# Kernel optimization log

Hardware: AMD Instinct MI355X
Metric: run time of the kernel (lower is better)

Reference implementation:

```python
import jax, jax.numpy as jnp
import numpy as np

N = 50000      # nodes
E = 800000     # edges
D_IN = 128
HID = 32
HEADS = 4
D_OUT = 64
NEG_SLOPE = 0.2  # DGL GATConv default


def gat_layer(feat, W, attn_l, attn_r, bias, src, dst, H, F):
    """One DGL-style GATConv layer. feat:[N,in], W:[in,H*F], attn:[H,F], bias:[H*F]."""
    n = feat.shape[0]
    hp = (feat @ W).reshape(n, H, F)                      # projected features [N,H,F]
    el = jnp.sum(hp * attn_l, axis=-1)                    # [N,H]
    er = jnp.sum(hp * attn_r, axis=-1)                    # [N,H]
    e = jax.nn.leaky_relu(el[src] + er[dst], NEG_SLOPE)   # per-edge score [E,H]
    # segment softmax over incoming edges of each dst node
    m = jax.ops.segment_max(e, dst, num_segments=n)       # [N,H]
    a = jnp.exp(e - m[dst])
    denom = jax.ops.segment_sum(a, dst, num_segments=n)   # [N,H]
    alpha = a / denom[dst]                                # [E,H]
    msg = alpha[:, :, None] * hp[src]                     # [E,H,F]
    out = jax.ops.segment_sum(msg, dst, num_segments=n)   # [N,H,F]
    return out + bias.reshape(1, H, F)


def setup_inputs() -> dict:
    key = jax.random.key(0)
    ks = jax.random.split(key, 12)
    s = 0.05
    x = jax.random.normal(ks[0], (N, D_IN), dtype=jnp.float32)
    src = jax.random.randint(ks[1], (E,), 0, N)
    dst = jax.random.randint(ks[2], (E,), 0, N)
    # layer 1: D_IN -> HID with HEADS heads
    W1 = jax.random.normal(ks[3], (D_IN, HEADS * HID), dtype=jnp.float32) * s
    al1 = jax.random.normal(ks[4], (HEADS, HID), dtype=jnp.float32) * s
    ar1 = jax.random.normal(ks[5], (HEADS, HID), dtype=jnp.float32) * s
    b1 = jnp.zeros((HEADS * HID,), dtype=jnp.float32)
    # layer 2: HID*HEADS -> D_OUT with 1 head
    W2 = jax.random.normal(ks[6], (HID * HEADS, D_OUT), dtype=jnp.float32) * s
    al2 = jax.random.normal(ks[7], (1, D_OUT), dtype=jnp.float32) * s
    ar2 = jax.random.normal(ks[8], (1, D_OUT), dtype=jnp.float32) * s
    b2 = jnp.zeros((D_OUT,), dtype=jnp.float32)
    return {"x": x, "W1": W1, "al1": al1, "ar1": ar1, "b1": b1,
            "W2": W2, "al2": al2, "ar2": ar2, "b2": b2,
            "src": src, "dst": dst}


def reference(x, W1, al1, ar1, b1, W2, al2, ar2, b2, src, dst):
    h1 = gat_layer(x, W1, al1, ar1, b1, src, dst, HEADS, HID)   # [N,HEADS,HID]
    h1 = h1.reshape(N, HEADS * HID)                              # concat heads
    h2 = gat_layer(h1, W2, al2, ar2, b2, src, dst, 1, D_OUT)     # [N,1,D_OUT]
    return h2.reshape(N, D_OUT)                                  # squeeze head dim
```

## Files before the change

kernel.cpp:

```cpp
#include <hip/hip_runtime.h>

#define NEG_SLOPE 0.2f

static __device__ __forceinline__ unsigned short f2bf(float f) {
  unsigned x = __float_as_uint(f);
  return (unsigned short)((x + 0x7FFFu + ((x >> 16) & 1u)) >> 16);
}
static __device__ __forceinline__ float bf2f(unsigned short u) {
  return __uint_as_float((unsigned)u << 16);
}

template<int NCOLS, int H>
__global__ __launch_bounds__(256) void gemm_eler_rank(const float* __restrict__ A,
    const float* __restrict__ B, const float* __restrict__ al, const float* __restrict__ ar,
    unsigned short* __restrict__ hb, float* __restrict__ el, float* __restrict__ er, int M,
    int gemmBlocks, const int* __restrict__ dst, int* deg, int* __restrict__ rank, int E) {
  constexpr int K = 128;
  constexpr int TM = 64;
  constexpr int F = NCOLS / H;
  __shared__ float As[TM][K];
  const int tid = threadIdx.x;

  if (blockIdx.x >= gemmBlocks) {
    const int e = (blockIdx.x - gemmBlocks) * 256 + tid;
    if (e < E) rank[e] = atomicAdd(&deg[dst[e]], 1);
    return;
  }

  const int m0 = blockIdx.x * TM;
  for (int i = tid; i < TM * K / 4; i += 256) {
    const int m = (i * 4) / K, k = (i * 4) % K;
    float4 v = make_float4(0.f, 0.f, 0.f, 0.f);
    if (m0 + m < M) v = *reinterpret_cast<const float4*>(&A[(size_t)(m0 + m) * K + k]);
    *reinterpret_cast<float4*>(&As[m][k]) = v;
  }
  __syncthreads();

  constexpr int CW = NCOLS / 32;
  const int c0 = (tid & 31) * CW;
  const int n0 = (tid >> 5) * 8;
  float acc[8][CW];
  #pragma unroll
  for (int i = 0; i < 8; ++i)
    #pragma unroll
    for (int j = 0; j < CW; ++j) acc[i][j] = 0.f;

  #pragma unroll 4
  for (int k = 0; k < K; ++k) {
    float wv[CW];
    if constexpr (CW == 4)
      *reinterpret_cast<float4*>(&wv[0]) = *reinterpret_cast<const float4*>(&B[(size_t)k * NCOLS + c0]);
    else
      *reinterpret_cast<float2*>(&wv[0]) = *reinterpret_cast<const float2*>(&B[(size_t)k * NCOLS + c0]);
    float xv[8];
    #pragma unroll
    for (int i = 0; i < 8; ++i) xv[i] = As[n0 + i][k];
    #pragma unroll
    for (int i = 0; i < 8; ++i)
      #pragma unroll
      for (int j = 0; j < CW; ++j)
        acc[i][j] = fmaf(xv[i], wv[j], acc[i][j]);
  }

  float alv[CW], arv[CW];
  if constexpr (CW == 4) {
    *reinterpret_cast<float4*>(&alv[0]) = *reinterpret_cast<const float4*>(&al[c0]);
    *reinterpret_cast<float4*>(&arv[0]) = *reinterpret_cast<const float4*>(&ar[c0]);
  } else {
    *reinterpret_cast<float2*>(&alv[0]) = *reinterpret_cast<const float2*>(&al[c0]);
    *reinterpret_cast<float2*>(&arv[0]) = *reinterpret_cast<const float2*>(&ar[c0]);
  }
  constexpr int GRP = F / CW;
  const int h = c0 / F;

  #pragma unroll
  for (int i = 0; i < 8; ++i) {
    const int m = m0 + n0 + i;
    if (m < M) {
      if constexpr (CW == 4) {
        ushort4 u;
        u.x = f2bf(acc[i][0]); u.y = f2bf(acc[i][1]);
        u.z = f2bf(acc[i][2]); u.w = f2bf(acc[i][3]);
        *reinterpret_cast<ushort4*>(&hb[(size_t)m * NCOLS + c0]) = u;
      } else {
        ushort2 u;
        u.x = f2bf(acc[i][0]); u.y = f2bf(acc[i][1]);
        *reinterpret_cast<ushort2*>(&hb[(size_t)m * NCOLS + c0]) = u;
      }
    }
    float pl = 0.f, pr = 0.f;
    #pragma unroll
    for (int j = 0; j < CW; ++j) {
      pl = fmaf(alv[j], acc[i][j], pl);
      pr = fmaf(arv[j], acc[i][j], pr);
    }
    #pragma unroll
    for (int off = 1; off < GRP; off <<= 1) {
      pl += __shfl_xor(pl, off);
      pr += __shfl_xor(pr, off);
    }
    if (((tid & 31) & (GRP - 1)) == 0 && m < M) {
      el[(size_t)m * H + h] = pl;
      er[(size_t)m * H + h] = pr;
    }
  }
}

__global__ __launch_bounds__(256) void block_sum_kernel(const int* __restrict__ deg,
    int* __restrict__ partials, int N) {
  __shared__ int wsum[4];
  const int tid = threadIdx.x;
  const int base = blockIdx.x * 1024 + tid * 4;
  int s = 0;
  #pragma unroll
  for (int j = 0; j < 4; ++j) if (base + j < N) s += deg[base + j];
  #pragma unroll
  for (int off = 32; off >= 1; off >>= 1) s += __shfl_down(s, off);
  if ((tid & 63) == 0) wsum[tid >> 6] = s;
  __syncthreads();
  if (tid == 0) partials[blockIdx.x] = wsum[0] + wsum[1] + wsum[2] + wsum[3];
}

__global__ __launch_bounds__(64) void scan_partials_kernel(int* partials, int nb) {
  const int tid = threadIdx.x;
  int v = (tid < nb) ? partials[tid] : 0;
  int incl = v;
  #pragma unroll
  for (int off = 1; off < 64; off <<= 1) {
    const int t = __shfl_up(incl, off);
    if (tid >= off) incl += t;
  }
  if (tid < nb) partials[tid] = incl - v;
}

__global__ __launch_bounds__(256) void block_scan_kernel(const int* __restrict__ deg,
    const int* __restrict__ partials, int* __restrict__ row_ptr, int N, int E) {
  __shared__ int wtot[4];
  const int tid = threadIdx.x;
  const int lane = tid & 63, wid = tid >> 6;
  const int idx = blockIdx.x * 1024 + tid * 4;
  int v[4];
  #pragma unroll
  for (int j = 0; j < 4; ++j) v[j] = (idx + j < N) ? deg[idx + j] : 0;
  const int tsum = v[0] + v[1] + v[2] + v[3];
  int incl = tsum;
  #pragma unroll
  for (int off = 1; off < 64; off <<= 1) {
    const int t = __shfl_up(incl, off);
    if (lane >= off) incl += t;
  }
  if (lane == 63) wtot[wid] = incl;
  __syncthreads();
  int excl = partials[blockIdx.x] + incl - tsum;
  for (int w = 0; w < wid; ++w) excl += wtot[w];
  #pragma unroll
  for (int j = 0; j < 4; ++j) {
    if (idx + j < N) { row_ptr[idx + j] = excl; excl += v[j]; }
  }
  if (blockIdx.x == 0 && tid == 0) row_ptr[N] = E;
}

__global__ __launch_bounds__(256) void place_kernel(const int* __restrict__ src,
    const int* __restrict__ dst, const int* __restrict__ row_ptr,
    const int* __restrict__ rank, unsigned short* __restrict__ csr_src, int E) {
  const int e = blockIdx.x * 256 + threadIdx.x;
  if (e < E) {
    csr_src[row_ptr[dst[e]] + rank[e]] = (unsigned short)src[e];
  }
}

template<int H, int F, int NPW>
__global__ __launch_bounds__(256) void gat_agg(const int* __restrict__ row_ptr,
    const unsigned short* __restrict__ csr_src, const float* __restrict__ el,
    const float* __restrict__ er, const unsigned short* __restrict__ hb,
    const float* __restrict__ bias, float* __restrict__ out, int N) {
  constexpr int HF = H * F;
  constexpr int LPN = 64 / NPW;
  constexpr int CPL = HF / LPN;
  static_assert(CPL == 4, "CPL must be 4");
  const int wid = threadIdx.x >> 6;
  const int lane = threadIdx.x & 63;
  const int g = lane / LPN;
  const int gl = lane % LPN;
  const int d = (blockIdx.x * 4 + wid) * NPW + g;
  if (d >= N) return;
  const int c0 = gl * CPL;
  const int h = c0 / F;
  const float erd = er[(size_t)d * H + h];
  const int beg = row_ptr[d], end = row_ptr[d + 1];
  float a0 = 0.f, a1 = 0.f, a2 = 0.f, a3 = 0.f, denom = 0.f;
  int i = beg;

  for (; i + 16 <= end; i += 16) {
    int s[16];
    #pragma unroll
    for (int j = 0; j < 16; ++j) s[j] = csr_src[i + j];
    float ee[16];
    #pragma unroll
    for (int j = 0; j < 16; ++j) ee[j] = el[(size_t)s[j] * H + h];
    ushort4 u[16];
    #pragma unroll
    for (int j = 0; j < 16; ++j)
      u[j] = *reinterpret_cast<const ushort4*>(&hb[(size_t)s[j] * HF + c0]);
    #pragma unroll
    for (int j = 0; j < 16; ++j) {
      float t = ee[j] + erd;
      t = fmaxf(t, NEG_SLOPE * t);
      const float x = __expf(t);
      denom += x;
      a0 = fmaf(x, bf2f(u[j].x), a0); a1 = fmaf(x, bf2f(u[j].y), a1);
      a2 = fmaf(x, bf2f(u[j].z), a2); a3 = fmaf(x, bf2f(u[j].w), a3);
    }
  }
  for (; i + 8 <= end; i += 8) {
    int s[8];
    #pragma unroll
    for (int j = 0; j < 8; ++j) s[j] = csr_src[i + j];
    float ee[8];
    #pragma unroll
    for (int j = 0; j < 8; ++j) ee[j] = el[(size_t)s[j] * H + h];
    ushort4 u[8];
    #pragma unroll
    for (int j = 0; j < 8; ++j)
      u[j] = *reinterpret_cast<const ushort4*>(&hb[(size_t)s[j] * HF + c0]);
    #pragma unroll
    for (int j = 0; j < 8; ++j) {
      float t = ee[j] + erd;
      t = fmaxf(t, NEG_SLOPE * t);
      const float x = __expf(t);
      denom += x;
      a0 = fmaf(x, bf2f(u[j].x), a0); a1 = fmaf(x, bf2f(u[j].y), a1);
      a2 = fmaf(x, bf2f(u[j].z), a2); a3 = fmaf(x, bf2f(u[j].w), a3);
    }
  }
  for (; i + 4 <= end; i += 4) {
    int s[4];
    #pragma unroll
    for (int j = 0; j < 4; ++j) s[j] = csr_src[i + j];
    float ee[4];
    #pragma unroll
    for (int j = 0; j < 4; ++j) ee[j] = el[(size_t)s[j] * H + h];
    ushort4 u[4];
    #pragma unroll
    for (int j = 0; j < 4; ++j)
      u[j] = *reinterpret_cast<const ushort4*>(&hb[(size_t)s[j] * HF + c0]);
    #pragma unroll
    for (int j = 0; j < 4; ++j) {
      float t = ee[j] + erd;
      t = fmaxf(t, NEG_SLOPE * t);
      const float x = __expf(t);
      denom += x;
      a0 = fmaf(x, bf2f(u[j].x), a0); a1 = fmaf(x, bf2f(u[j].y), a1);
      a2 = fmaf(x, bf2f(u[j].z), a2); a3 = fmaf(x, bf2f(u[j].w), a3);
    }
  }
  for (; i < end; ++i) {
    const int s = csr_src[i];
    float t = el[(size_t)s * H + h] + erd;
    t = fmaxf(t, NEG_SLOPE * t);
    const float x = __expf(t);
    denom += x;
    const ushort4 u = *reinterpret_cast<const ushort4*>(&hb[(size_t)s * HF + c0]);
    a0 = fmaf(x, bf2f(u.x), a0); a1 = fmaf(x, bf2f(u.y), a1);
    a2 = fmaf(x, bf2f(u.z), a2); a3 = fmaf(x, bf2f(u.w), a3);
  }

  const float inv = denom > 0.f ? 1.f / denom : 0.f;
  const float4 bv = *reinterpret_cast<const float4*>(&bias[c0]);
  float4 o;
  o.x = bv.x + a0 * inv; o.y = bv.y + a1 * inv;
  o.z = bv.z + a2 * inv; o.w = bv.w + a3 * inv;
  *reinterpret_cast<float4*>(&out[(size_t)d * HF + c0]) = o;
}

extern "C" void kernel_launch(void* const* d_in, const int* in_sizes, int n_in,
                              void* d_out, int out_size, void* d_ws, size_t ws_size,
                              hipStream_t stream) {
  const float* x   = (const float*)d_in[0];
  const float* W1  = (const float*)d_in[1];
  const float* al1 = (const float*)d_in[2];
  const float* ar1 = (const float*)d_in[3];
  const float* b1  = (const float*)d_in[4];
  const float* W2  = (const float*)d_in[5];
  const float* al2 = (const float*)d_in[6];
  const float* ar2 = (const float*)d_in[7];
  const float* b2  = (const float*)d_in[8];
  const int* src   = (const int*)d_in[9];
  const int* dst   = (const int*)d_in[10];
  const int N = in_sizes[0] / 128;
  const int E = in_sizes[9];
  float* out = (float*)d_out;

  float* ws   = (float*)d_ws;
  float* out1 = ws;
  float* el1  = out1 + (size_t)N * 128;
  float* er1  = el1 + (size_t)N * 4;
  float* el2  = er1 + (size_t)N * 4;
  float* er2  = el2 + N;
  int* deg     = (int*)(er2 + N);
  int* row_ptr = deg + N;
  int* rank    = row_ptr + N + 1;
  unsigned short* csr_src = (unsigned short*)(rank + E);
  int* partials = (int*)(csr_src + ((E + 1) & ~1));
  unsigned short* hb1 = (unsigned short*)(partials + 64);
  unsigned short* hb2 = hb1 + (size_t)N * 128;

  const dim3 blk(256);
  const int nb = (N + 1023) / 1024;
  const int gemmBlocks = (N + 63) / 64;
  const int rankBlocks = (E + 255) / 256;

  hipMemsetAsync(deg, 0, (size_t)N * sizeof(int), stream);
  gemm_eler_rank<128, 4><<<dim3(gemmBlocks + rankBlocks), blk, 0, stream>>>(
      x, W1, al1, ar1, hb1, el1, er1, N, gemmBlocks, dst, deg, rank, E);

  block_sum_kernel<<<dim3(nb), blk, 0, stream>>>(deg, partials, N);
  scan_partials_kernel<<<dim3(1), dim3(64), 0, stream>>>(partials, nb);
  block_scan_kernel<<<dim3(nb), blk, 0, stream>>>(deg, partials, row_ptr, N, E);
  place_kernel<<<dim3(rankBlocks), blk, 0, stream>>>(src, dst, row_ptr, rank, csr_src, E);

  gat_agg<4, 32, 2><<<dim3((N + 7) / 8), blk, 0, stream>>>(row_ptr, csr_src, el1, er1, hb1, b1, out1, N);

  gemm_eler_rank<64, 1><<<dim3(gemmBlocks), blk, 0, stream>>>(
      out1, W2, al2, ar2, hb2, el2, er2, N, gemmBlocks, dst, deg, rank, 0);
  gat_agg<1, 64, 4><<<dim3((N + 15) / 16), blk, 0, stream>>>(row_ptr, csr_src, el2, er2, hb2, b2, out, N);
}
```

Measured before the change: 168.6 us.

## Move GAT projections to bf16 MFMA and store layer-1 output as bf16

Replaces the scalar fp32 FMA GEMMs with bf16 MFMA 16x16x32 GEMMs. A new prep kernel packs W1 and W2 into MFMA fragment layout and also does the edge-rank atomics with 8 edges per thread. Layer-1 el/er are now computed inside the CSR placement kernel from the bf16 projection, and the layer-1 aggregation writes bf16 so the second GEMM reads half the bytes. The cost is lower precision (bf16 inputs, bf16 intermediate activations) and el1/er1 built from rounded features.

```diff
diff --git a/kernel.cpp b/kernel.cpp
--- a/kernel.cpp
+++ b/kernel.cpp
@@ -1,6 +1,9 @@
 #include <hip/hip_runtime.h>
 
 #define NEG_SLOPE 0.2f
+
+typedef __attribute__((ext_vector_type(8))) short bf16x8;
+typedef __attribute__((ext_vector_type(4))) float f32x4;
 
 static __device__ __forceinline__ unsigned short f2bf(float f) {
   unsigned x = __float_as_uint(f);
@@ -10,98 +13,134 @@
   return __uint_as_float((unsigned)u << 16);
 }
 
-template<int NCOLS, int H>
-__global__ __launch_bounds__(256) void gemm_eler_rank(const float* __restrict__ A,
-    const float* __restrict__ B, const float* __restrict__ al, const float* __restrict__ ar,
-    unsigned short* __restrict__ hb, float* __restrict__ el, float* __restrict__ er, int M,
-    int gemmBlocks, const int* __restrict__ dst, int* deg, int* __restrict__ rank, int E) {
-  constexpr int K = 128;
-  constexpr int TM = 64;
-  constexpr int F = NCOLS / H;
-  __shared__ float As[TM][K];
-  const int tid = threadIdx.x;
-
-  if (blockIdx.x >= gemmBlocks) {
-    const int e = (blockIdx.x - gemmBlocks) * 256 + tid;
-    if (e < E) rank[e] = atomicAdd(&deg[dst[e]], 1);
+__global__ __launch_bounds__(256) void prep_kernel(const float* __restrict__ W1,
+    const float* __restrict__ W2, unsigned short* __restrict__ Bp1,
+    unsigned short* __restrict__ Bp2, const int* __restrict__ src,
+    const int* __restrict__ dst, int* deg, int* __restrict__ rank, int E, int rankBlocks) {
+  const int tid = threadIdx.x;
+  if (blockIdx.x < rankBlocks) {
+    const int base = blockIdx.x * 2048 + tid;
+    int e[8], dv[8], r[8];
+    #pragma unroll
+    for (int b = 0; b < 8; ++b) e[b] = base + b * 256;
+    #pragma unroll
+    for (int b = 0; b < 8; ++b) if (e[b] < E) dv[b] = dst[e[b]];
+    #pragma unroll
+    for (int b = 0; b < 8; ++b) if (e[b] < E) r[b] = atomicAdd(&deg[dv[b]], 1);
+    #pragma unroll
+    for (int b = 0; b < 8; ++b) if (e[b] < E) rank[e[b]] = r[b];
     return;
   }
-
-  const int m0 = blockIdx.x * TM;
-  for (int i = tid; i < TM * K / 4; i += 256) {
-    const int m = (i * 4) / K, k = (i * 4) % K;
-    float4 v = make_float4(0.f, 0.f, 0.f, 0.f);
-    if (m0 + m < M) v = *reinterpret_cast<const float4*>(&A[(size_t)(m0 + m) * K + k]);
-    *reinterpret_cast<float4*>(&As[m][k]) = v;
+  const int pb = blockIdx.x - rankBlocks;
+  const int lane = tid & 63, warp = tid >> 6;
+  const int k0 = (lane >> 4) * 8;
+  const int cl = lane & 15;
+  if (pb == 0) {
+    for (int f = warp; f < 32; f += 4) {
+      const int ct = f >> 2, ks = f & 3;
+      const int c = ct * 16 + cl;
+      unsigned short t[8];
+      #pragma unroll
+      for (int j = 0; j < 8; ++j) t[j] = f2bf(W1[(ks * 32 + k0 + j) * 128 + c]);
+      #pragma unroll
+      for (int j = 0; j < 8; ++j) Bp1[((size_t)f * 64 + lane) * 8 + j] = t[j];
+    }
+  } else if (pb == 1) {
+    for (int f = warp; f < 16; f += 4) {
+      const int ct = f >> 2, ks = f & 3;
+      const int c = ct * 16 + cl;
+      unsigned short t[8];
+      #pragma unroll
+      for (int j = 0; j < 8; ++j) t[j] = f2bf(W2[(ks * 32 + k0 + j) * 64 + c]);
+      #pragma unroll
+      for (int j = 0; j < 8; ++j) Bp2[((size_t)f * 64 + lane) * 8 + j] = t[j];
+    }
+  }
+}
+
+template<int NT, bool AFP32, bool ELER>
+__global__ __launch_bounds__(256) void gemm_mfma(const void* __restrict__ Asrc,
+    const unsigned short* __restrict__ Bp, const float* __restrict__ al,
+    const float* __restrict__ ar, unsigned short* __restrict__ hb,
+    float* __restrict__ el, float* __restrict__ er, int M) {
+  constexpr int CT = NT / 16;
+  constexpr int LDA = 136;
+  __shared__ unsigned short As[64][LDA];
+  const int tid = threadIdx.x;
+  const int m0 = blockIdx.x * 64;
+
+  {
+    const int r = tid >> 2, q = tid & 3;
+    const int m = m0 + r;
+    if constexpr (AFP32) {
+      const float* A = (const float*)Asrc;
+      #pragma unroll
+      for (int i = 0; i < 8; ++i) {
+        float4 v = make_float4(0.f, 0.f, 0.f, 0.f);
+        if (m < M) v = *reinterpret_cast<const float4*>(&A[(size_t)m * 128 + q * 32 + i * 4]);
+        ushort4 u;
+        u.x = f2bf(v.x); u.y = f2bf(v.y); u.z = f2bf(v.z); u.w = f2bf(v.w);
+        *reinterpret_cast<ushort4*>(&As[r][q * 32 + i * 4]) = u;
+      }
+    } else {
+      const unsigned short* A = (const unsigned short*)Asrc;
+      #pragma unroll
+      for (int i = 0; i < 4; ++i) {
+        ulonglong2 v = make_ulonglong2(0, 0);
+        if (m < M) v = *reinterpret_cast<const ulonglong2*>(&A[(size_t)m * 128 + q * 32 + i * 8]);
+        *reinterpret_cast<ulonglong2*>(&As[r][q * 32 + i * 8]) = v;
+      }
+    }
   }
   __syncthreads();
 
-  constexpr int CW = NCOLS / 32;
-  const int c0 = (tid & 31) * CW;
-  const int n0 = (tid >> 5) * 8;
-  float acc[8][CW];
-  #pragma unroll
-  for (int i = 0; i < 8; ++i)
-    #pragma unroll
-    for (int j = 0; j < CW; ++j) acc[i][j] = 0.f;
-
-  #pragma unroll 4
-  for (int k = 0; k < K; ++k) {
-    float wv[CW];
-    if constexpr (CW == 4)
-      *reinterpret_cast<float4*>(&wv[0]) = *reinterpret_cast<const float4*>(&B[(size_t)k * NCOLS + c0]);
-    else
-      *reinterpret_cast<float2*>(&wv[0]) = *reinterpret_cast<const float2*>(&B[(size_t)k * NCOLS + c0]);
-    float xv[8];
-    #pragma unroll
-    for (int i = 0; i < 8; ++i) xv[i] = As[n0 + i][k];
-    #pragma unroll
-    for (int i = 0; i < 8; ++i)
-      #pragma unroll
-      for (int j = 0; j < CW; ++j)
-        acc[i][j] = fmaf(xv[i], wv[j], acc[i][j]);
-  }
-
-  float alv[CW], arv[CW];
-  if constexpr (CW == 4) {
-    *reinterpret_cast<float4*>(&alv[0]) = *reinterpret_cast<const float4*>(&al[c0]);
-    *reinterpret_cast<float4*>(&arv[0]) = *reinterpret_cast<const float4*>(&ar[c0]);
-  } else {
-    *reinterpret_cast<float2*>(&alv[0]) = *reinterpret_cast<const float2*>(&al[c0]);
-    *reinterpret_cast<float2*>(&arv[0]) = *reinterpret_cast<const float2*>(&ar[c0]);
-  }
-  constexpr int GRP = F / CW;
-  const int h = c0 / F;
-
-  #pragma unroll
-  for (int i = 0; i < 8; ++i) {
-    const int m = m0 + n0 + i;
-    if (m < M) {
-      if constexpr (CW == 4) {
-        ushort4 u;
-        u.x = f2bf(acc[i][0]); u.y = f2bf(acc[i][1]);
-        u.z = f2bf(acc[i][2]); u.w = f2bf(acc[i][3]);
-        *reinterpret_cast<ushort4*>(&hb[(size_t)m * NCOLS + c0]) = u;
-      } else {
-        ushort2 u;
-        u.x = f2bf(acc[i][0]); u.y = f2bf(acc[i][1]);
-        *reinterpret_cast<ushort2*>(&hb[(size_t)m * NCOLS + c0]) = u;
+  const int w = tid >> 6, lane = tid & 63;
+  const int arow = w * 16 + (lane & 15);
+  const int koff = (lane >> 4) * 8;
+  f32x4 acc[CT];
+  #pragma unroll
+  for (int ct = 0; ct < CT; ++ct) acc[ct] = (f32x4){0.f, 0.f, 0.f, 0.f};
+
+  #pragma unroll
+  for (int ks = 0; ks < 4; ++ks) {
+    const bf16x8 af = *reinterpret_cast<const bf16x8*>(&As[arow][ks * 32 + koff]);
+    #pragma unroll
+    for (int ct = 0; ct < CT; ++ct) {
+      const bf16x8 bfr = *reinterpret_cast<const bf16x8*>(&Bp[((size_t)(ct * 4 + ks) * 64 + lane) * 8]);
+      acc[ct] = __builtin_amdgcn_mfma_f32_16x16x32_bf16(af, bfr, acc[ct], 0, 0, 0);
+    }
+  }
+
+  const int rbase = m0 + w * 16 + (lane >> 4) * 4;
+  const int cl = lane & 15;
+  #pragma unroll
+  for (int ct = 0; ct < CT; ++ct) {
+    const int c = ct * 16 + cl;
+    #pragma unroll
+    for (int reg = 0; reg < 4; ++reg) {
+      const int m = rbase + reg;
+      if (m < M) hb[(size_t)m * NT + c] = f2bf(acc[ct][reg]);
+    }
+  }
+  if constexpr (ELER) {
+    float alv[CT], arv[CT];
+    #pragma unroll
+    for (int ct = 0; ct < CT; ++ct) { alv[ct] = al[ct * 16 + cl]; arv[ct] = ar[ct * 16 + cl]; }
+    #pragma unroll
+    for (int reg = 0; reg < 4; ++reg) {
+      float pl = 0.f, pr = 0.f;
+      #pragma unroll
+      for (int ct = 0; ct < CT; ++ct) {
+        pl = fmaf(alv[ct], acc[ct][reg], pl);
+        pr = fmaf(arv[ct], acc[ct][reg], pr);
       }
-    }
-    float pl = 0.f, pr = 0.f;
-    #pragma unroll
-    for (int j = 0; j < CW; ++j) {
-      pl = fmaf(alv[j], acc[i][j], pl);
-      pr = fmaf(arv[j], acc[i][j], pr);
-    }
-    #pragma unroll
-    for (int off = 1; off < GRP; off <<= 1) {
-      pl += __shfl_xor(pl, off);
-      pr += __shfl_xor(pr, off);
-    }
-    if (((tid & 31) & (GRP - 1)) == 0 && m < M) {
-      el[(size_t)m * H + h] = pl;
-      er[(size_t)m * H + h] = pr;
+      #pragma unroll
+      for (int off = 1; off < 16; off <<= 1) {
+        pl += __shfl_xor(pl, off);
+        pr += __shfl_xor(pr, off);
+      }
+      const int m = rbase + reg;
+      if (cl == 0 && m < M) { el[m] = pl; er[m] = pr; }
     }
   }
 }
@@ -160,20 +199,37 @@
   if (blockIdx.x == 0 && tid == 0) row_ptr[N] = E;
 }
 
-__global__ __launch_bounds__(256) void place_kernel(const int* __restrict__ src,
+__global__ __launch_bounds__(256) void place_eler_kernel(const int* __restrict__ src,
     const int* __restrict__ dst, const int* __restrict__ row_ptr,
-    const int* __restrict__ rank, unsigned short* __restrict__ csr_src, int E) {
-  const int e = blockIdx.x * 256 + threadIdx.x;
-  if (e < E) {
-    csr_src[row_ptr[dst[e]] + rank[e]] = (unsigned short)src[e];
-  }
-}
-
-template<int H, int F, int NPW>
+    const int* __restrict__ rank, unsigned short* __restrict__ csr_src, int E,
+    int placeBlocks, const unsigned short* __restrict__ hb1,
+    const float* __restrict__ al1, const float* __restrict__ ar1,
+    float* __restrict__ el1, float* __restrict__ er1, int N) {
+  const int tid = threadIdx.x;
+  if (blockIdx.x < placeBlocks) {
+    const int e = blockIdx.x * 256 + tid;
+    if (e < E) csr_src[row_ptr[dst[e]] + rank[e]] = (unsigned short)src[e];
+    return;
+  }
+  const int idx = (blockIdx.x - placeBlocks) * 256 + tid;
+  if (idx >= N * 4) return;
+  const int h = idx & 3;
+  const unsigned short* row = hb1 + (size_t)(idx >> 2) * 128 + h * 32;
+  float sl = 0.f, sr = 0.f;
+  #pragma unroll
+  for (int f = 0; f < 32; ++f) {
+    const float v = bf2f(row[f]);
+    sl = fmaf(al1[h * 32 + f], v, sl);
+    sr = fmaf(ar1[h * 32 + f], v, sr);
+  }
+  el1[idx] = sl; er1[idx] = sr;
+}
+
+template<int H, int F, int NPW, bool OBF>
 __global__ __launch_bounds__(256) void gat_agg(const int* __restrict__ row_ptr,
     const unsigned short* __restrict__ csr_src, const float* __restrict__ el,
     const float* __restrict__ er, const unsigned short* __restrict__ hb,
-    const float* __restrict__ bias, float* __restrict__ out, int N) {
+    const float* __restrict__ bias, void* __restrict__ outp, int N) {
   constexpr int HF = H * F;
   constexpr int LPN = 64 / NPW;
   constexpr int CPL = HF / LPN;
@@ -267,10 +323,17 @@
 
   const float inv = denom > 0.f ? 1.f / denom : 0.f;
   const float4 bv = *reinterpret_cast<const float4*>(&bias[c0]);
-  float4 o;
-  o.x = bv.x + a0 * inv; o.y = bv.y + a1 * inv;
-  o.z = bv.z + a2 * inv; o.w = bv.w + a3 * inv;
-  *reinterpret_cast<float4*>(&out[(size_t)d * HF + c0]) = o;
+  if constexpr (OBF) {
+    ushort4 o;
+    o.x = f2bf(bv.x + a0 * inv); o.y = f2bf(bv.y + a1 * inv);
+    o.z = f2bf(bv.z + a2 * inv); o.w = f2bf(bv.w + a3 * inv);
+    *reinterpret_cast<ushort4*>(&((unsigned short*)outp)[(size_t)d * HF + c0]) = o;
+  } else {
+    float4 o;
+    o.x = bv.x + a0 * inv; o.y = bv.y + a1 * inv;
+    o.z = bv.z + a2 * inv; o.w = bv.w + a3 * inv;
+    *reinterpret_cast<float4*>(&((float*)outp)[(size_t)d * HF + c0]) = o;
+  }
 }
 
 extern "C" void kernel_launch(void* const* d_in, const int* in_sizes, int n_in,
@@ -291,37 +354,51 @@
   const int E = in_sizes[9];
   float* out = (float*)d_out;
 
-  float* ws   = (float*)d_ws;
-  float* out1 = ws;
-  float* el1  = out1 + (size_t)N * 128;
-  float* er1  = el1 + (size_t)N * 4;
-  float* el2  = er1 + (size_t)N * 4;
-  float* er2  = el2 + N;
-  int* deg     = (int*)(er2 + N);
-  int* row_ptr = deg + N;
-  int* rank    = row_ptr + N + 1;
-  unsigned short* csr_src = (unsigned short*)(rank + E);
-  int* partials = (int*)(csr_src + ((E + 1) & ~1));
-  unsigned short* hb1 = (unsigned short*)(partials + 64);
-  unsigned short* hb2 = hb1 + (size_t)N * 128;
+  char* wp = (char*)d_ws;
+  auto alloc = [&wp](size_t bytes) {
+    char* r = wp;
+    wp += (bytes + 31) & ~size_t(31);
+    return r;
+  };
+  float* el1  = (float*)alloc((size_t)N * 4 * sizeof(float));
+  float* er1  = (float*)alloc((size_t)N * 4 * sizeof(float));
+  float* el2  = (float*)alloc((size_t)N * sizeof(float));
+  float* er2  = (float*)alloc((size_t)N * sizeof(float));
+  int* deg     = (int*)alloc((size_t)N * sizeof(int));
+  int* row_ptr = (int*)alloc((size_t)(N + 1) * sizeof(int));
+  int* rank    = (int*)alloc((size_t)E * sizeof(int));
+  int* partials = (int*)alloc(64 * sizeof(int));
+  unsigned short* csr_src = (unsigned short*)alloc((size_t)E * sizeof(unsigned short));
+  unsigned short* out1b   = (unsigned short*)alloc((size_t)N * 128 * sizeof(unsigned short));
+  unsigned short* hb1     = (unsigned short*)alloc((size_t)N * 128 * sizeof(unsigned short));
+  unsigned short* hb2     = (unsigned short*)alloc((size_t)N * 64 * sizeof(unsigned short));
+  unsigned short* Bp1     = (unsigned short*)alloc(128 * 128 * sizeof(unsigned short));
+  unsigned short* Bp2     = (unsigned short*)alloc(128 * 64 * sizeof(unsigned short));
 
   const dim3 blk(256);
   const int nb = (N + 1023) / 1024;
   const int gemmBlocks = (N + 63) / 64;
-  const int rankBlocks = (E + 255) / 256;
+  const int rankBlocks = (E + 2047) / 2048;
+  const int placeBlocks = (E + 255) / 256;
+  const int elerBlocks = (N * 4 + 255) / 256;
 
   hipMemsetAsync(deg, 0, (size_t)N * sizeof(int), stream);
-  gemm_eler_rank<128, 4><<<dim3(gemmBlocks + rankBlocks), blk, 0, stream>>>(
-      x, W1, al1, ar1, hb1, el1, er1, N, gemmBlocks, dst, deg, rank, E);
+  prep_kernel<<<dim3(rankBlocks + 2), blk, 0, stream>>>(W1, W2, Bp1, Bp2, src, dst, deg, rank, E, rankBlocks);
+
+  gemm_mfma<128, true, false><<<dim3(gemmBlocks), blk, 0, stream>>>(
+      x, Bp1, nullptr, nullptr, hb1, nullptr, nullptr, N);
 
   block_sum_kernel<<<dim3(nb), blk, 0, stream>>>(deg, partials, N);
   scan_partials_kernel<<<dim3(1), dim3(64), 0, stream>>>(partials, nb);
   block_scan_kernel<<<dim3(nb), blk, 0, stream>>>(deg, partials, row_ptr, N, E);
-  place_kernel<<<dim3(rankBlocks), blk, 0, stream>>>(src, dst, row_ptr, rank, csr_src, E);
-
-  gat_agg<4, 32, 2><<<dim3((N + 7) / 8), blk, 0, stream>>>(row_ptr, csr_src, el1, er1, hb1, b1, out1, N);
-
-  gemm_eler_rank<64, 1><<<dim3(gemmBlocks), blk, 0, stream>>>(
-      out1, W2, al2, ar2, hb2, el2, er2, N, gemmBlocks, dst, deg, rank, 0);
-  gat_agg<1, 64, 4><<<dim3((N + 15) / 16), blk, 0, stream>>>(row_ptr, csr_src, el2, er2, hb2, b2, out, N);
-}
+  place_eler_kernel<<<dim3(placeBlocks + elerBlocks), blk, 0, stream>>>(
+      src, dst, row_ptr, rank, csr_src, E, placeBlocks, hb1, al1, ar1, el1, er1, N);
+
+  gat_agg<4, 32, 2, true><<<dim3((N + 7) / 8), blk, 0, stream>>>(
+      row_ptr, csr_src, el1, er1, hb1, b1, out1b, N);
+
+  gemm_mfma<64, false, true><<<dim3(gemmBlocks), blk, 0, stream>>>(
+      out1b, Bp2, al2, ar2, hb2, el2, er2, N);
+  gat_agg<1, 64, 4, false><<<dim3((N + 15) / 16), blk, 0, stream>>>(
+      row_ptr, csr_src, el2, er2, hb2, b2, out, N);
+}
```

Result: faster. 164.8 us (-2.2%).
